# Optimization experiments

Hardware: AMD Instinct MI355X
Metric: run time of the kernel (lower is better)

Reference implementation:

```python
import jax, jax.numpy as jnp
import numpy as np

N_NODES = 100000


def _prep(edge_index, n, dtype):
    # Add self-loops and compute GCN symmetric normalization (edge_weight = 1).
    loop = jnp.arange(n)
    src = jnp.concatenate([edge_index[0], loop])
    dst = jnp.concatenate([edge_index[1], loop])
    ones = jnp.ones(src.shape[0], dtype)
    deg = jax.ops.segment_sum(ones, dst, num_segments=n)  # in-degree over col, incl. self-loop
    dinv = jnp.where(deg > 0, 1.0 / jnp.sqrt(deg), 0.0)
    norm = dinv[src] * dinv[dst]  # per-edge deg^-1/2 * deg^-1/2
    cnt = jnp.maximum(deg, 1.0)   # incoming-edge count for aggr='mean' (weights are 1)
    return src, dst, norm, cnt


def _gcn_conv(h, W, b, src, dst, norm, cnt, n):
    # gather -> scale -> scatter-mean  (PyG GCNConv with aggr='mean')
    msg = norm[:, None] * (h @ W)[src]                      # [E+N, out]
    agg = jax.ops.segment_sum(msg, dst, num_segments=n)     # [N, out]
    return agg / cnt[:, None] + b


def setup_inputs() -> dict:
    key = jax.random.key(0)
    ks = jax.random.split(key, 8)
    n, d_in, d_h, d_out = N_NODES, 128, 128, 64
    x = jax.random.normal(ks[0], (n, d_in), dtype=jnp.float32)
    edge_index = jax.random.randint(ks[1], (2, 1600000), 0, n, dtype=jnp.int64)
    def glorot(k, fan_in, fan_out):
        s = jnp.sqrt(6.0 / (fan_in + fan_out)).astype(jnp.float32)
        return jax.random.uniform(k, (fan_in, fan_out), jnp.float32, -s, s)
    return {
        "x": x,
        "edge_index": edge_index,
        "W1": glorot(ks[2], d_in, d_h), "b1": jnp.zeros((d_h,), jnp.float32),
        "W2": glorot(ks[3], d_h, d_h), "b2": jnp.zeros((d_h,), jnp.float32),
        "W3": glorot(ks[4], d_h, d_out), "b3": jnp.zeros((d_out,), jnp.float32),
    }


def reference(x, edge_index, W1, b1, W2, b2, W3, b3):
    n = x.shape[0]
    src, dst, norm, cnt = _prep(edge_index, n, x.dtype)
    h = jax.nn.relu(_gcn_conv(x, W1, b1, src, dst, norm, cnt, n))  # dropout = identity (eval)
    h = jax.nn.relu(_gcn_conv(h, W2, b2, src, dst, norm, cnt, n))
    out = _gcn_conv(h, W3, b3, src, dst, norm, cnt, n)
    return out
```

## Files before the change

### kernel.cpp

```cpp
#include <hip/hip_runtime.h>
#include <hip/hip_fp16.h>
#include <math.h>


#define BLK 256

typedef short bf16x8 __attribute__((ext_vector_type(8)));
typedef float f32x4 __attribute__((ext_vector_type(4)));

__device__ __forceinline__ unsigned short f2bf(float f) {
    unsigned int u = __float_as_uint(f);
    u += 0x7fffu + ((u >> 16) & 1u);
    return (unsigned short)(u >> 16);
}

__device__ __forceinline__ int sel4(const int4 v, int q) {
    return (q == 0) ? v.x : (q == 1) ? v.y : (q == 2) ? v.z : v.w;
}

__device__ __forceinline__ void acc8(float* __restrict__ acc, const __half* __restrict__ p) {
    uint4 u = *(const uint4*)p;
    const __half2* h = (const __half2*)&u;
    float2 f0 = __half22float2(h[0]);
    float2 f1 = __half22float2(h[1]);
    float2 f2 = __half22float2(h[2]);
    float2 f3 = __half22float2(h[3]);
    acc[0] += f0.x; acc[1] += f0.y; acc[2] += f1.x; acc[3] += f1.y;
    acc[4] += f2.x; acc[5] += f2.y; acc[6] += f3.x; acc[7] += f3.y;
}

__global__ __launch_bounds__(256) void megaA(
    const int* __restrict__ dst, int* __restrict__ deg, int* __restrict__ rnk, int E,
    int* __restrict__ colidx, int Epad, int n,
    const float* __restrict__ W1, const float* __restrict__ W2, const float* __restrict__ W3,
    unsigned short* __restrict__ Wt1, unsigned short* __restrict__ Wt2,
    unsigned short* __restrict__ Wt3, int nCount, int nInit) {
    const int b = blockIdx.x, t = threadIdx.x;
    if (b < nCount) {
        int stride = nCount * 256;
        for (int e = b * 256 + t; e < E; e += stride)
            rnk[e] = atomicAdd(&deg[dst[e]], 1);
    } else if (b < nCount + nInit) {
        int bb = b - nCount;
        int4* c4 = (int4*)colidx;
        const int len4 = Epad >> 2;
        int4 v = make_int4(n, n, n, n);
        for (int i = bb * 256 + t; i < len4; i += nInit * 256) c4[i] = v;
    } else {
        int idx = (b - nCount - nInit) * 256 + t;
        if (idx < 16384) {
            int k = idx >> 7, c = idx & 127;
            Wt1[c * 128 + k] = f2bf(W1[idx]);
        } else if (idx < 32768) {
            int j = idx - 16384; int k = j >> 7, c = j & 127;
            Wt2[c * 128 + k] = f2bf(W2[j]);
        } else if (idx < 40960) {
            int j = idx - 32768; int k = j >> 6, c = j & 63;
            Wt3[c * 128 + k] = f2bf(W3[j]);
        }
    }
}

__global__ void scan_block_sums(const int* __restrict__ deg, int* __restrict__ bsum, int n) {
    __shared__ int s[BLK];
    int i = blockIdx.x * BLK + threadIdx.x;
    s[threadIdx.x] = (i < n) ? ((deg[i] + 7) & ~7) : 0;
    __syncthreads();
    for (int off = BLK / 2; off > 0; off >>= 1) {
        if (threadIdx.x < off) s[threadIdx.x] += s[threadIdx.x + off];
        __syncthreads();
    }
    if (threadIdx.x == 0) bsum[blockIdx.x] = s[0];
}

__global__ void scan_partials_excl(int* __restrict__ bsum, int nb) {
    __shared__ int a[512];
    __shared__ int b[512];
    int t = threadIdx.x;
    int v = (t < nb) ? bsum[t] : 0;
    a[t] = v;
    __syncthreads();
    int* s = a; int* d = b;
    for (int off = 1; off < 512; off <<= 1) {
        int val = s[t];
        if (t >= off) val += s[t - off];
        d[t] = val;
        __syncthreads();
        int* tmp = s; s = d; d = tmp;
    }
    if (t < nb) bsum[t] = s[t] - v;
}

__global__ void scan_write_rowptr(const int* __restrict__ deg, const int* __restrict__ bsum,
                                  int* __restrict__ rowptr, float* __restrict__ dinv, int n) {
    __shared__ int a[BLK];
    __shared__ int b[BLK];
    int t = threadIdx.x;
    int i = blockIdx.x * BLK + t;
    int dgv = (i < n) ? deg[i] : 0;
    int v = (i < n) ? ((dgv + 7) & ~7) : 0;
    a[t] = v;
    __syncthreads();
    int* s = a; int* d = b;
    for (int off = 1; off < BLK; off <<= 1) {
        int val = s[t];
        if (t >= off) val += s[t - off];
        d[t] = val;
        __syncthreads();
        int* tmp = s; s = d; d = tmp;
    }
    if (i < n) {
        rowptr[i] = (s[t] - v) + bsum[blockIdx.x];
        dinv[i] = rsqrtf((float)(dgv + 1));
    }
}

template <int KOUT, bool HF32, bool FOLD>
__device__ __forceinline__ void gemm_body(int gb, const void* __restrict__ Hv,
                                          const unsigned short* __restrict__ Wt,
                                          const float* __restrict__ dinv,
                                          __half* __restrict__ Y, int n,
                                          unsigned short (*Hl)[72],
                                          unsigned short (*Wl)[72]) {
    const int t = threadIdx.x;
    const int row0 = gb * 64;
    const int wave = t >> 6, lane = t & 63;
    const int r16 = lane & 15, ko8 = (lane >> 4) * 8;

    if (gb == 0 && t < KOUT) Y[(size_t)n * KOUT + t] = __float2half(0.f);

    f32x4 acc[KOUT / 16];
#pragma unroll
    for (int c = 0; c < KOUT / 16; c++) acc[c] = (f32x4){0.f, 0.f, 0.f, 0.f};

#pragma unroll
    for (int h = 0; h < 2; h++) {
        if (h) __syncthreads();
        for (int idx = t; idx < KOUT * 8; idx += 256) {
            int r = idx >> 3, seg = idx & 7;
            *(uint4*)&Wl[r][seg * 8] = *(const uint4*)(Wt + r * 128 + h * 64 + seg * 8);
        }
        if (HF32) {
            const float* H = (const float*)Hv;
            for (int idx = t; idx < 64 * 8; idx += 256) {
                int r = idx >> 3, seg = idx & 7;
                int row = row0 + r;
                unsigned short tmp[8];
                if (row < n) {
                    const float* p = H + (size_t)row * 128 + h * 64 + seg * 8;
                    float4 v0 = *(const float4*)p, v1 = *(const float4*)(p + 4);
                    tmp[0] = f2bf(v0.x); tmp[1] = f2bf(v0.y); tmp[2] = f2bf(v0.z); tmp[3] = f2bf(v0.w);
                    tmp[4] = f2bf(v1.x); tmp[5] = f2bf(v1.y); tmp[6] = f2bf(v1.z); tmp[7] = f2bf(v1.w);
                } else {
#pragma unroll
                    for (int j = 0; j < 8; j++) tmp[j] = 0;
                }
                *(uint4*)&Hl[r][seg * 8] = *(const uint4*)tmp;
            }
        } else {
            const unsigned short* H = (const unsigned short*)Hv;
            for (int idx = t; idx < 64 * 8; idx += 256) {
                int r = idx >> 3, seg = idx & 7;
                int row = row0 + r;
                uint4 v = make_uint4(0, 0, 0, 0);
                if (row < n) v = *(const uint4*)(H + (size_t)row * 128 + h * 64 + seg * 8);
                *(uint4*)&Hl[r][seg * 8] = v;
            }
        }
        __syncthreads();
#pragma unroll
        for (int kc = 0; kc < 2; kc++) {
            bf16x8 a = *(const bf16x8*)&Hl[wave * 16 + r16][kc * 32 + ko8];
#pragma unroll
            for (int c = 0; c < KOUT / 16; c++) {
                bf16x8 bb = *(const bf16x8*)&Wl[c * 16 + r16][kc * 32 + ko8];
                acc[c] = __builtin_amdgcn_mfma_f32_16x16x32_bf16(a, bb, acc[c], 0, 0, 0);
            }
        }
    }

    const int mbase = row0 + wave * 16 + (lane >> 4) * 4;
#pragma unroll
    for (int r = 0; r < 4; r++) {
        int row = mbase + r;
        if (row < n) {
            float dv = FOLD ? dinv[row] : 1.f;
#pragma unroll
            for (int c = 0; c < KOUT / 16; c++)
                Y[(size_t)row * KOUT + c * 16 + r16] = __float2half_rn(acc[c][r] * dv);
        }
    }
}

__global__ __launch_bounds__(256) void megaB(
    const int* __restrict__ src, const int* __restrict__ dst,
    const int* __restrict__ rnk, const int* __restrict__ rowptr,
    int* __restrict__ colidx, int E,
    const float* __restrict__ x, const unsigned short* __restrict__ Wt1,
    const float* __restrict__ dinv, __half* __restrict__ Y, int n, int nPlace) {
    __shared__ unsigned short Hl[64][72];
    __shared__ unsigned short Wl[128][72];
    const int b = blockIdx.x, t = threadIdx.x;
    if (b < nPlace) {
        int stride = nPlace * 256;
        for (int e = b * 256 + t; e < E; e += stride)
            colidx[rowptr[dst[e]] + rnk[e]] = src[e];
    } else {
        gemm_body<128, true, true>(b - nPlace, x, Wt1, dinv, Y, n, Hl, Wl);
    }
}

template <int KOUT>
__global__ __launch_bounds__(256) void gemm_std(const unsigned short* __restrict__ H,
                                                const unsigned short* __restrict__ Wt,
                                                __half* __restrict__ Y, int n) {
    __shared__ unsigned short Hl[64][72];
    __shared__ unsigned short Wl[KOUT][72];
    gemm_body<KOUT, false, false>(blockIdx.x, H, Wt, nullptr, Y, n, Hl, Wl);
}

__global__ __launch_bounds__(256) void agg128(const __half* __restrict__ Ys,
                                              const int* __restrict__ deg,
                                              const float* __restrict__ dinv,
                                              const int* __restrict__ rowptr,
                                              const int* __restrict__ colidx,
                                              const float* __restrict__ bias,
                                              unsigned short* __restrict__ outb, int n) {
    int wid = (blockIdx.x * blockDim.x + threadIdx.x) >> 6;
    int lane = threadIdx.x & 63;
    if (wid >= n) return;
    const int q = lane >> 4;
    const int l4 = lane & 15;

    int start = __builtin_amdgcn_readfirstlane(rowptr[wid]);
    int m     = __builtin_amdgcn_readfirstlane(deg[wid]);
    int mpad  = (m + 7) & ~7;
    float di = dinv[wid];

    float acc[8];
#pragma unroll
    for (int j = 0; j < 8; j++) acc[j] = 0.f;
    if (q == 0) acc8(acc, Ys + ((size_t)wid << 7) + l4 * 8);

    const int4* cp4 = (const int4*)(colidx + start);
    for (int j = 0; j < mpad; j += 8) {
        int4 a = cp4[j >> 2];
        int4 b = cp4[(j >> 2) + 1];
        int s0 = sel4(a, q), s1 = sel4(b, q);
        acc8(acc, Ys + ((size_t)s0 << 7) + l4 * 8);
        acc8(acc, Ys + ((size_t)s1 << 7) + l4 * 8);
    }
#pragma unroll
    for (int j = 0; j < 8; j++) {
        acc[j] += __shfl_xor(acc[j], 16);
        acc[j] += __shfl_xor(acc[j], 32);
    }

    if (q == 0) {
        float scale = di / (float)(m + 1);
        float4 b0 = *(const float4*)(bias + l4 * 8);
        float4 b1 = *(const float4*)(bias + l4 * 8 + 4);
        float o[8];
        o[0] = acc[0] * scale + b0.x; o[1] = acc[1] * scale + b0.y;
        o[2] = acc[2] * scale + b0.z; o[3] = acc[3] * scale + b0.w;
        o[4] = acc[4] * scale + b1.x; o[5] = acc[5] * scale + b1.y;
        o[6] = acc[6] * scale + b1.z; o[7] = acc[7] * scale + b1.w;
        unsigned short ob[8];
#pragma unroll
        for (int j = 0; j < 8; j++) ob[j] = f2bf(fmaxf(o[j], 0.f) * di);
        *(uint4*)(outb + ((size_t)wid << 7) + l4 * 8) = *(const uint4*)ob;
    }
}

__global__ __launch_bounds__(256) void agg64(const __half* __restrict__ Ys,
                                             const int* __restrict__ deg,
                                             const float* __restrict__ dinv,
                                             const int* __restrict__ rowptr,
                                             const int* __restrict__ colidx,
                                             const float* __restrict__ bias,
                                             float* __restrict__ out, int n) {
    int wid = (blockIdx.x * blockDim.x + threadIdx.x) >> 6;
    int lane = threadIdx.x & 63;
    if (wid >= n) return;
    const int oct = lane >> 3;
    const int l3 = lane & 7;

    int start = __builtin_amdgcn_readfirstlane(rowptr[wid]);
    int m     = __builtin_amdgcn_readfirstlane(deg[wid]);
    int mpad  = (m + 7) & ~7;
    float di = dinv[wid];

    float acc[8];
#pragma unroll
    for (int j = 0; j < 8; j++) acc[j] = 0.f;
    if (oct == 0) acc8(acc, Ys + ((size_t)wid << 6) + l3 * 8);

    const int4* cp4 = (const int4*)(colidx + start);
    for (int j = 0; j < mpad; j += 8) {
        int4 a = cp4[j >> 2];
        int4 b = cp4[(j >> 2) + 1];
        int se = (oct < 4) ? sel4(a, oct) : sel4(b, oct - 4);
        acc8(acc, Ys + ((size_t)se << 6) + l3 * 8);
    }
#pragma unroll
    for (int j = 0; j < 8; j++) {
        acc[j] += __shfl_xor(acc[j], 8);
        acc[j] += __shfl_xor(acc[j], 16);
        acc[j] += __shfl_xor(acc[j], 32);
    }

    if (oct == 0) {
        float scale = di / (float)(m + 1);
        float4 b0 = *(const float4*)(bias + l3 * 8);
        float4 b1 = *(const float4*)(bias + l3 * 8 + 4);
        float o[8];
        o[0] = acc[0] * scale + b0.x; o[1] = acc[1] * scale + b0.y;
        o[2] = acc[2] * scale + b0.z; o[3] = acc[3] * scale + b0.w;
        o[4] = acc[4] * scale + b1.x; o[5] = acc[5] * scale + b1.y;
        o[6] = acc[6] * scale + b1.z; o[7] = acc[7] * scale + b1.w;
        float* op = out + ((size_t)wid << 6) + l3 * 8;
        *(float4*)op = make_float4(o[0], o[1], o[2], o[3]);
        *(float4*)(op + 4) = make_float4(o[4], o[5], o[6], o[7]);
    }
}

extern "C" void kernel_launch(void* const* d_in, const int* in_sizes, int n_in,
                              void* d_out, int out_size, void* d_ws, size_t ws_size,
                              hipStream_t stream) {
    const float* x  = (const float*)d_in[0];
    const int*   ei = (const int*)d_in[1];
    const float* W1 = (const float*)d_in[2];
    const float* b1 = (const float*)d_in[3];
    const float* W2 = (const float*)d_in[4];
    const float* b2 = (const float*)d_in[5];
    const float* W3 = (const float*)d_in[6];
    const float* b3 = (const float*)d_in[7];
    float* out = (float*)d_out;

    const int n = in_sizes[0] / 128;
    const int E = in_sizes[1] / 2;
    const int* srcA = ei;
    const int* dstA = ei + E;
    const int Epad = E + 8 * n + 64;

    auto alignup = [](size_t v) { return (v + 255) & ~(size_t)255; };
    char* base = (char*)d_ws;
    size_t off = 0;
    int* deg    = (int*)(base + off); off = alignup(off + (size_t)n * 4);
    int* rnk    = (int*)(base + off); off = alignup(off + (size_t)E * 4);
    int* rowptr = (int*)(base + off); off = alignup(off + (size_t)n * 4);
    int* bsum   = (int*)(base + off); off = alignup(off + (size_t)1024 * 4);
    int* colidx = (int*)(base + off); off = alignup(off + (size_t)Epad * 4);
    float* dinv = (float*)(base + off); off = alignup(off + (size_t)n * 4);
    unsigned short* Wt1 = (unsigned short*)(base + off); off = alignup(off + 16384 * 2);
    unsigned short* Wt2 = (unsigned short*)(base + off); off = alignup(off + 16384 * 2);
    unsigned short* Wt3 = (unsigned short*)(base + off); off = alignup(off + 8192 * 2);
    unsigned short* Hb  = (unsigned short*)(base + off); off = alignup(off + (size_t)n * 128 * 2);
    __half* Yb  = (__half*)(base + off); off = alignup(off + (size_t)(n + 1) * 128 * 2);
    (void)ws_size;

    const int nbN = (n + BLK - 1) / BLK;
    const int nCount = 512, nInit = 256, nCast = 160;
    const int nPlace = 512;
    const int nGemm = (n + 63) / 64;
    const int aggBlocks = (n * 64 + BLK - 1) / BLK;

    hipMemsetAsync(deg, 0, (size_t)n * 4, stream);

    megaA<<<nCount + nInit + nCast, 256, 0, stream>>>(
        dstA, deg, rnk, E, colidx, Epad, n, W1, W2, W3, Wt1, Wt2, Wt3, nCount, nInit);

    scan_block_sums<<<nbN, BLK, 0, stream>>>(deg, bsum, n);
    scan_partials_excl<<<1, 512, 0, stream>>>(bsum, nbN);
    scan_write_rowptr<<<nbN, BLK, 0, stream>>>(deg, bsum, rowptr, dinv, n);

    megaB<<<nPlace + nGemm, 256, 0, stream>>>(
        srcA, dstA, rnk, rowptr, colidx, E, x, Wt1, dinv, Yb, n, nPlace);

    agg128<<<aggBlocks, BLK, 0, stream>>>(Yb, deg, dinv, rowptr, colidx, b1, Hb, n);

    gemm_std<128><<<nGemm, 256, 0, stream>>>(Hb, Wt2, Yb, n);
    agg128<<<aggBlocks, BLK, 0, stream>>>(Yb, deg, dinv, rowptr, colidx, b2, Hb, n);

    gemm_std<64><<<nGemm, 256, 0, stream>>>(Hb, Wt3, Yb, n);
    agg64<<<aggBlocks, BLK, 0, stream>>>(Yb, deg, dinv, rowptr, colidx, b3, out, n);
}
```

Baseline: 337.3 us.

## Store GEMM output in column-sliced layout and aggregate per 16-column slice

The GEMM now writes Y as column slices of 16 halfs per node ([slice][n+1][16]) instead of row-major. Aggregation kernels assign one slice per block and two lanes per node, so each node's gather touches a compact 32-byte row within a slice that is small enough to stay cache-resident, in place of whole rows spread across memory. This also removes the cross-lane shuffle reduction, at the cost of re-reading colidx once per slice and giving each thread a serial loop over the node's degree. The count-block number in megaA is also raised.

```diff
diff --git a/kernel.cpp b/kernel.cpp
--- a/kernel.cpp
+++ b/kernel.cpp
@@ -12,10 +12,6 @@
     unsigned int u = __float_as_uint(f);
     u += 0x7fffu + ((u >> 16) & 1u);
     return (unsigned short)(u >> 16);
-}
-
-__device__ __forceinline__ int sel4(const int4 v, int q) {
-    return (q == 0) ? v.x : (q == 1) ? v.y : (q == 2) ? v.z : v.w;
 }
 
 __device__ __forceinline__ void acc8(float* __restrict__ acc, const __half* __restrict__ p) {
@@ -127,7 +123,8 @@
     const int wave = t >> 6, lane = t & 63;
     const int r16 = lane & 15, ko8 = (lane >> 4) * 8;
 
-    if (gb == 0 && t < KOUT) Y[(size_t)n * KOUT + t] = __float2half(0.f);
+    if (gb == 0 && t < KOUT)
+        Y[((size_t)(t >> 4) * (n + 1) + n) * 16 + (t & 15)] = __float2half(0.f);
 
     f32x4 acc[KOUT / 16];
 #pragma unroll
@@ -187,7 +184,7 @@
             float dv = FOLD ? dinv[row] : 1.f;
 #pragma unroll
             for (int c = 0; c < KOUT / 16; c++)
-                Y[(size_t)row * KOUT + c * 16 + r16] = __float2half_rn(acc[c][r] * dv);
+                Y[((size_t)c * (n + 1) + row) * 16 + r16] = __float2half_rn(acc[c][r] * dv);
         }
     }
 }
@@ -225,51 +222,43 @@
                                               const int* __restrict__ rowptr,
                                               const int* __restrict__ colidx,
                                               const float* __restrict__ bias,
-                                              unsigned short* __restrict__ outb, int n) {
-    int wid = (blockIdx.x * blockDim.x + threadIdx.x) >> 6;
-    int lane = threadIdx.x & 63;
-    if (wid >= n) return;
-    const int q = lane >> 4;
-    const int l4 = lane & 15;
-
-    int start = __builtin_amdgcn_readfirstlane(rowptr[wid]);
-    int m     = __builtin_amdgcn_readfirstlane(deg[wid]);
-    int mpad  = (m + 7) & ~7;
-    float di = dinv[wid];
+                                              unsigned short* __restrict__ Hb, int n) {
+    const int bid = blockIdx.x;
+    const int slice = bid & 7;
+    const int wave = threadIdx.x >> 6, lane = threadIdx.x & 63;
+    const int g = lane >> 1, p = lane & 1;
+    const int node = (bid >> 3) * 128 + wave * 32 + g;
+    if (node >= n) return;
+    const __half* Ysl = Ys + (size_t)slice * (n + 1) * 16;
+
+    int m     = deg[node];
+    int start = rowptr[node];
+    float di  = dinv[node];
+    int mpad  = (m + 3) & ~3;
 
     float acc[8];
 #pragma unroll
     for (int j = 0; j < 8; j++) acc[j] = 0.f;
-    if (q == 0) acc8(acc, Ys + ((size_t)wid << 7) + l4 * 8);
-
-    const int4* cp4 = (const int4*)(colidx + start);
-    for (int j = 0; j < mpad; j += 8) {
-        int4 a = cp4[j >> 2];
-        int4 b = cp4[(j >> 2) + 1];
-        int s0 = sel4(a, q), s1 = sel4(b, q);
-        acc8(acc, Ys + ((size_t)s0 << 7) + l4 * 8);
-        acc8(acc, Ys + ((size_t)s1 << 7) + l4 * 8);
-    }
+    acc8(acc, Ysl + (size_t)node * 16 + p * 8);
+
+    const int* cp = colidx + start;
+    for (int j = 0; j < mpad; j += 4) {
+        int4 e = *(const int4*)(cp + j);
+        acc8(acc, Ysl + (size_t)e.x * 16 + p * 8);
+        acc8(acc, Ysl + (size_t)e.y * 16 + p * 8);
+        acc8(acc, Ysl + (size_t)e.z * 16 + p * 8);
+        acc8(acc, Ysl + (size_t)e.w * 16 + p * 8);
+    }
+
+    float scale = di / (float)(m + 1);
+    int cb = slice * 16 + p * 8;
+    unsigned short ob[8];
 #pragma unroll
     for (int j = 0; j < 8; j++) {
-        acc[j] += __shfl_xor(acc[j], 16);
-        acc[j] += __shfl_xor(acc[j], 32);
-    }
-
-    if (q == 0) {
-        float scale = di / (float)(m + 1);
-        float4 b0 = *(const float4*)(bias + l4 * 8);
-        float4 b1 = *(const float4*)(bias + l4 * 8 + 4);
-        float o[8];
-        o[0] = acc[0] * scale + b0.x; o[1] = acc[1] * scale + b0.y;
-        o[2] = acc[2] * scale + b0.z; o[3] = acc[3] * scale + b0.w;
-        o[4] = acc[4] * scale + b1.x; o[5] = acc[5] * scale + b1.y;
-        o[6] = acc[6] * scale + b1.z; o[7] = acc[7] * scale + b1.w;
-        unsigned short ob[8];
-#pragma unroll
-        for (int j = 0; j < 8; j++) ob[j] = f2bf(fmaxf(o[j], 0.f) * di);
-        *(uint4*)(outb + ((size_t)wid << 7) + l4 * 8) = *(const uint4*)ob;
-    }
+        float o = acc[j] * scale + bias[cb + j];
+        ob[j] = f2bf(fmaxf(o, 0.f) * di);
+    }
+    *(uint4*)(Hb + (size_t)node * 128 + cb) = *(const uint4*)ob;
 }
 
 __global__ __launch_bounds__(256) void agg64(const __half* __restrict__ Ys,
@@ -279,49 +268,43 @@
                                              const int* __restrict__ colidx,
                                              const float* __restrict__ bias,
                                              float* __restrict__ out, int n) {
-    int wid = (blockIdx.x * blockDim.x + threadIdx.x) >> 6;
-    int lane = threadIdx.x & 63;
-    if (wid >= n) return;
-    const int oct = lane >> 3;
-    const int l3 = lane & 7;
-
-    int start = __builtin_amdgcn_readfirstlane(rowptr[wid]);
-    int m     = __builtin_amdgcn_readfirstlane(deg[wid]);
-    int mpad  = (m + 7) & ~7;
-    float di = dinv[wid];
+    const int bid = blockIdx.x;
+    const int slice = bid & 3;
+    const int wave = threadIdx.x >> 6, lane = threadIdx.x & 63;
+    const int g = lane >> 1, p = lane & 1;
+    const int node = (bid >> 2) * 128 + wave * 32 + g;
+    if (node >= n) return;
+    const __half* Ysl = Ys + (size_t)slice * (n + 1) * 16;
+
+    int m     = deg[node];
+    int start = rowptr[node];
+    float di  = dinv[node];
+    int mpad  = (m + 3) & ~3;
 
     float acc[8];
 #pragma unroll
     for (int j = 0; j < 8; j++) acc[j] = 0.f;
-    if (oct == 0) acc8(acc, Ys + ((size_t)wid << 6) + l3 * 8);
-
-    const int4* cp4 = (const int4*)(colidx + start);
-    for (int j = 0; j < mpad; j += 8) {
-        int4 a = cp4[j >> 2];
-        int4 b = cp4[(j >> 2) + 1];
-        int se = (oct < 4) ? sel4(a, oct) : sel4(b, oct - 4);
-        acc8(acc, Ys + ((size_t)se << 6) + l3 * 8);
-    }
-#pragma unroll
-    for (int j = 0; j < 8; j++) {
-        acc[j] += __shfl_xor(acc[j], 8);
-        acc[j] += __shfl_xor(acc[j], 16);
-        acc[j] += __shfl_xor(acc[j], 32);
-    }
-
-    if (oct == 0) {
-        float scale = di / (float)(m + 1);
-        float4 b0 = *(const float4*)(bias + l3 * 8);
-        float4 b1 = *(const float4*)(bias + l3 * 8 + 4);
-        float o[8];
-        o[0] = acc[0] * scale + b0.x; o[1] = acc[1] * scale + b0.y;
-        o[2] = acc[2] * scale + b0.z; o[3] = acc[3] * scale + b0.w;
-        o[4] = acc[4] * scale + b1.x; o[5] = acc[5] * scale + b1.y;
-        o[6] = acc[6] * scale + b1.z; o[7] = acc[7] * scale + b1.w;
-        float* op = out + ((size_t)wid << 6) + l3 * 8;
-        *(float4*)op = make_float4(o[0], o[1], o[2], o[3]);
-        *(float4*)(op + 4) = make_float4(o[4], o[5], o[6], o[7]);
-    }
+    acc8(acc, Ysl + (size_t)node * 16 + p * 8);
+
+    const int* cp = colidx + start;
+    for (int j = 0; j < mpad; j += 4) {
+        int4 e = *(const int4*)(cp + j);
+        acc8(acc, Ysl + (size_t)e.x * 16 + p * 8);
+        acc8(acc, Ysl + (size_t)e.y * 16 + p * 8);
+        acc8(acc, Ysl + (size_t)e.z * 16 + p * 8);
+        acc8(acc, Ysl + (size_t)e.w * 16 + p * 8);
+    }
+
+    float scale = di / (float)(m + 1);
+    int cb = slice * 16 + p * 8;
+    float4 o0, o1;
+    o0.x = acc[0] * scale + bias[cb];     o0.y = acc[1] * scale + bias[cb + 1];
+    o0.z = acc[2] * scale + bias[cb + 2]; o0.w = acc[3] * scale + bias[cb + 3];
+    o1.x = acc[4] * scale + bias[cb + 4]; o1.y = acc[5] * scale + bias[cb + 5];
+    o1.z = acc[6] * scale + bias[cb + 6]; o1.w = acc[7] * scale + bias[cb + 7];
+    float* op = out + (size_t)node * 64 + cb;
+    *(float4*)op = o0;
+    *(float4*)(op + 4) = o1;
 }
 
 extern "C" void kernel_launch(void* const* d_in, const int* in_sizes, int n_in,
@@ -360,10 +343,10 @@
     (void)ws_size;
 
     const int nbN = (n + BLK - 1) / BLK;
-    const int nCount = 512, nInit = 256, nCast = 160;
+    const int nCount = 2048, nInit = 256, nCast = 160;
     const int nPlace = 512;
     const int nGemm = (n + 63) / 64;
-    const int aggBlocks = (n * 64 + BLK - 1) / BLK;
+    const int nChunk = (n + 127) / 128;
 
     hipMemsetAsync(deg, 0, (size_t)n * 4, stream);
 
@@ -377,11 +360,11 @@
     megaB<<<nPlace + nGemm, 256, 0, stream>>>(
         srcA, dstA, rnk, rowptr, colidx, E, x, Wt1, dinv, Yb, n, nPlace);
 
-    agg128<<<aggBlocks, BLK, 0, stream>>>(Yb, deg, dinv, rowptr, colidx, b1, Hb, n);
+    agg128<<<8 * nChunk, BLK, 0, stream>>>(Yb, deg, dinv, rowptr, colidx, b1, Hb, n);
 
     gemm_std<128><<<nGemm, 256, 0, stream>>>(Hb, Wt2, Yb, n);
-    agg128<<<aggBlocks, BLK, 0, stream>>>(Yb, deg, dinv, rowptr, colidx, b2, Hb, n);
+    agg128<<<8 * nChunk, BLK, 0, stream>>>(Yb, deg, dinv, rowptr, colidx, b2, Hb, n);
 
     gemm_std<64><<<nGemm, 256, 0, stream>>>(Hb, Wt3, Yb, n);
-    agg64<<<aggBlocks, BLK, 0, stream>>>(Yb, deg, dinv, rowptr, colidx, b3, out, n);
-}
+    agg64<<<4 * nChunk, BLK, 0, stream>>>(Yb, deg, dinv, rowptr, colidx, b3, out, n);
+}
```

After: 383.6 us. 1.14x slower.
